# Kernel tuning notes

Measured on AMD Instinct MI355X. Metric: run time of the kernel, lower is better.

The kernel has to match this reference:

```python
import jax, jax.numpy as jnp
import numpy as np


def setup_inputs() -> dict:
    key = jax.random.key(0)
    k1, k2 = jax.random.split(key)
    B, C, H, W, T = 32, 128, 16, 16, 32
    outputs = jax.random.normal(k1, (B, C, H, W, T), dtype=jnp.float32)
    target = (jax.random.uniform(k2, (B, C, H, W, T)) < 0.2).astype(jnp.float32)
    return {"outputs": outputs, "target": target, "n_steps": T, "tau_s": 4}


def _psp(target, tau_s):
    """Leaky integrator over the last (time) axis: syn_t = syn_{t-1}*(1-1/tau) + x_t; out_t = syn_t/tau."""
    tau = jnp.asarray(tau_s, target.dtype)
    decay = 1.0 - 1.0 / tau
    x = jnp.moveaxis(target, -1, 0)  # [T, B, C, H, W]

    def step(syn, x_t):
        syn = syn * decay + x_t
        return syn, syn / tau

    _, syns = jax.lax.scan(step, jnp.zeros(target.shape[:-1], target.dtype), x)
    return jnp.moveaxis(syns, 0, -1)  # [B, C, H, W, T]


def reference(outputs, target, n_steps, tau_s):
    # spike_kernel: delta = outputs - psp(target); loss = 0.5 * sum(delta^2)
    target_psp = _psp(target, tau_s)
    delta = outputs - target_psp
    return 0.5 * jnp.sum(delta * delta)
```

## Files before the change

### kernel.cpp

```cpp
#include <hip/hip_runtime.h>


#define NBLOCKS 2048
#define NTHREADS 256

__global__ __launch_bounds__(NTHREADS) void spike_loss_main(
    const float* __restrict__ outputs,
    const float* __restrict__ target,
    const int* __restrict__ tau_p,
    float* __restrict__ partials,
    int total4)
{
    const float tau = (float)tau_p[0];
    const float d  = 1.0f - 1.0f / tau;
    const float inv_tau = 1.0f / tau;
    const float d2 = d * d;
    const float d3 = d2 * d;
    const float d4 = d2 * d2;
    const float d8 = d4 * d4;
    const float d16 = d8 * d8;

    const int lane = threadIdx.x & 63;
    const int j = lane & 7;

    const float4* __restrict__ t4 = (const float4*)target;
    const float4* __restrict__ o4 = (const float4*)outputs;

    float acc = 0.0f;
    const int stride = gridDim.x * blockDim.x;
    for (int g = blockIdx.x * blockDim.x + threadIdx.x; g < total4; g += stride) {
        float4 x = t4[g];

        float s0 = x.x;
        float s1 = s0 * d + x.y;
        float s2 = s1 * d + x.z;
        float s3 = s2 * d + x.w;

        float S = s3;
        float u;
        u = __shfl_up(S, 1, 8); S += (j >= 1) ? d4  * u : 0.0f;
        u = __shfl_up(S, 2, 8); S += (j >= 2) ? d8  * u : 0.0f;
        u = __shfl_up(S, 4, 8); S += (j >= 4) ? d16 * u : 0.0f;

        float cp = __shfl_up(S, 1, 8);
        cp = (j >= 1) ? cp : 0.0f;
        s0 += cp * d;
        s1 += cp * d2;
        s2 += cp * d3;
        s3 += cp * d4;

        float4 o = o4[g];
        float e0 = o.x - s0 * inv_tau;
        float e1 = o.y - s1 * inv_tau;
        float e2 = o.z - s2 * inv_tau;
        float e3 = o.w - s3 * inv_tau;
        acc += e0 * e0 + e1 * e1 + e2 * e2 + e3 * e3;
    }

    #pragma unroll
    for (int o = 32; o > 0; o >>= 1) acc += __shfl_down(acc, o, 64);

    __shared__ float wsum[NTHREADS / 64];
    if (lane == 0) wsum[threadIdx.x >> 6] = acc;
    __syncthreads();
    if (threadIdx.x == 0) {
        float s = 0.0f;
        #pragma unroll
        for (int w = 0; w < NTHREADS / 64; ++w) s += wsum[w];
        partials[blockIdx.x] = s;
    }
}

__global__ __launch_bounds__(NTHREADS) void spike_loss_final(
    const float* __restrict__ partials, float* __restrict__ out, int n)
{
    float acc = 0.0f;
    for (int i = threadIdx.x; i < n; i += NTHREADS) acc += partials[i];
    #pragma unroll
    for (int o = 32; o > 0; o >>= 1) acc += __shfl_down(acc, o, 64);

    __shared__ float wsum[NTHREADS / 64];
    const int lane = threadIdx.x & 63;
    if (lane == 0) wsum[threadIdx.x >> 6] = acc;
    __syncthreads();
    if (threadIdx.x == 0) {
        float s = 0.0f;
        #pragma unroll
        for (int w = 0; w < NTHREADS / 64; ++w) s += wsum[w];
        out[0] = 0.5f * s;
    }
}

extern "C" void kernel_launch(void* const* d_in, const int* in_sizes, int n_in,
                              void* d_out, int out_size, void* d_ws, size_t ws_size,
                              hipStream_t stream) {
    const float* outputs = (const float*)d_in[0];
    const float* target  = (const float*)d_in[1];
    const int*   tau_p   = (const int*)d_in[3];

    float* partials = (float*)d_ws;
    const int total4 = in_sizes[0] / 4;

    spike_loss_main<<<NBLOCKS, NTHREADS, 0, stream>>>(outputs, target, tau_p, partials, total4);
    spike_loss_final<<<1, NTHREADS, 0, stream>>>(partials, (float*)d_out, NBLOCKS);
}
```

Measured before the change: 51.71 us.

## Unroll loads 8-deep and fuse final reduction via atomicAdd

Batches eight float4 loads per tensor ahead of the scan arithmetic, using a scheduling barrier, to raise memory-level parallelism. It replaces the second reduction kernel with a per-block atomicAdd into the output, which is zeroed by a memset, and turns the lane masks into precomputed FMA weights. This saves a kernel launch and keeps more loads in flight, at the cost of higher register use and a result that depends on the order of atomic additions.

```diff
diff --git a/kernel.cpp b/kernel.cpp
--- a/kernel.cpp
+++ b/kernel.cpp
@@ -3,12 +3,13 @@
 
 #define NBLOCKS 2048
 #define NTHREADS 256
+#define U 8
 
-__global__ __launch_bounds__(NTHREADS) void spike_loss_main(
+__global__ __launch_bounds__(NTHREADS) void spike_loss_fused(
     const float* __restrict__ outputs,
     const float* __restrict__ target,
     const int* __restrict__ tau_p,
-    float* __restrict__ partials,
+    float* __restrict__ out,
     int total4)
 {
     const float tau = (float)tau_p[0];
@@ -23,38 +24,79 @@
     const int lane = threadIdx.x & 63;
     const int j = lane & 7;
 
+    const float w1 = (j >= 1) ? d4  : 0.0f;
+    const float w2 = (j >= 2) ? d8  : 0.0f;
+    const float w4 = (j >= 4) ? d16 : 0.0f;
+    const float c1 = (j >= 1) ? d   : 0.0f;
+    const float c2 = (j >= 1) ? d2  : 0.0f;
+    const float c3 = (j >= 1) ? d3  : 0.0f;
+    const float c4 = (j >= 1) ? d4  : 0.0f;
+
     const float4* __restrict__ t4 = (const float4*)target;
     const float4* __restrict__ o4 = (const float4*)outputs;
 
     float acc = 0.0f;
     const int stride = gridDim.x * blockDim.x;
-    for (int g = blockIdx.x * blockDim.x + threadIdx.x; g < total4; g += stride) {
-        float4 x = t4[g];
+    int g = blockIdx.x * blockDim.x + threadIdx.x;
 
+    for (; g + (U - 1) * stride < total4; g += U * stride) {
+        float4 xv[U], ov[U];
+        #pragma unroll
+        for (int u = 0; u < U; ++u) xv[u] = t4[g + u * stride];
+        #pragma unroll
+        for (int u = 0; u < U; ++u) ov[u] = o4[g + u * stride];
+        __builtin_amdgcn_sched_barrier(0);
+
+        #pragma unroll
+        for (int u = 0; u < U; ++u) {
+            float4 x = xv[u], o = ov[u];
+            float s0 = x.x;
+            float s1 = s0 * d + x.y;
+            float s2 = s1 * d + x.z;
+            float s3 = s2 * d + x.w;
+            float S = s3;
+            float u1 = __shfl_up(S, 1, 8); S = fmaf(w1, u1, S);
+            float u2 = __shfl_up(S, 2, 8); S = fmaf(w2, u2, S);
+            float u4 = __shfl_up(S, 4, 8); S = fmaf(w4, u4, S);
+            float cp = __shfl_up(S, 1, 8);
+            s0 = fmaf(cp, c1, s0);
+            s1 = fmaf(cp, c2, s1);
+            s2 = fmaf(cp, c3, s2);
+            s3 = fmaf(cp, c4, s3);
+
+            float e0 = fmaf(-inv_tau, s0, o.x);
+            float e1 = fmaf(-inv_tau, s1, o.y);
+            float e2 = fmaf(-inv_tau, s2, o.z);
+            float e3 = fmaf(-inv_tau, s3, o.w);
+            acc = fmaf(e0, e0, acc);
+            acc = fmaf(e1, e1, acc);
+            acc = fmaf(e2, e2, acc);
+            acc = fmaf(e3, e3, acc);
+        }
+    }
+    for (; g < total4; g += stride) {
+        float4 x = t4[g], o = o4[g];
         float s0 = x.x;
         float s1 = s0 * d + x.y;
         float s2 = s1 * d + x.z;
         float s3 = s2 * d + x.w;
-
         float S = s3;
-        float u;
-        u = __shfl_up(S, 1, 8); S += (j >= 1) ? d4  * u : 0.0f;
-        u = __shfl_up(S, 2, 8); S += (j >= 2) ? d8  * u : 0.0f;
-        u = __shfl_up(S, 4, 8); S += (j >= 4) ? d16 * u : 0.0f;
-
+        float u1 = __shfl_up(S, 1, 8); S = fmaf(w1, u1, S);
+        float u2 = __shfl_up(S, 2, 8); S = fmaf(w2, u2, S);
+        float u4 = __shfl_up(S, 4, 8); S = fmaf(w4, u4, S);
         float cp = __shfl_up(S, 1, 8);
-        cp = (j >= 1) ? cp : 0.0f;
-        s0 += cp * d;
-        s1 += cp * d2;
-        s2 += cp * d3;
-        s3 += cp * d4;
-
-        float4 o = o4[g];
-        float e0 = o.x - s0 * inv_tau;
-        float e1 = o.y - s1 * inv_tau;
-        float e2 = o.z - s2 * inv_tau;
-        float e3 = o.w - s3 * inv_tau;
-        acc += e0 * e0 + e1 * e1 + e2 * e2 + e3 * e3;
+        s0 = fmaf(cp, c1, s0);
+        s1 = fmaf(cp, c2, s1);
+        s2 = fmaf(cp, c3, s2);
+        s3 = fmaf(cp, c4, s3);
+        float e0 = fmaf(-inv_tau, s0, o.x);
+        float e1 = fmaf(-inv_tau, s1, o.y);
+        float e2 = fmaf(-inv_tau, s2, o.z);
+        float e3 = fmaf(-inv_tau, s3, o.w);
+        acc = fmaf(e0, e0, acc);
+        acc = fmaf(e1, e1, acc);
+        acc = fmaf(e2, e2, acc);
+        acc = fmaf(e3, e3, acc);
     }
 
     #pragma unroll
@@ -67,27 +109,7 @@
         float s = 0.0f;
         #pragma unroll
         for (int w = 0; w < NTHREADS / 64; ++w) s += wsum[w];
-        partials[blockIdx.x] = s;
-    }
-}
-
-__global__ __launch_bounds__(NTHREADS) void spike_loss_final(
-    const float* __restrict__ partials, float* __restrict__ out, int n)
-{
-    float acc = 0.0f;
-    for (int i = threadIdx.x; i < n; i += NTHREADS) acc += partials[i];
-    #pragma unroll
-    for (int o = 32; o > 0; o >>= 1) acc += __shfl_down(acc, o, 64);
-
-    __shared__ float wsum[NTHREADS / 64];
-    const int lane = threadIdx.x & 63;
-    if (lane == 0) wsum[threadIdx.x >> 6] = acc;
-    __syncthreads();
-    if (threadIdx.x == 0) {
-        float s = 0.0f;
-        #pragma unroll
-        for (int w = 0; w < NTHREADS / 64; ++w) s += wsum[w];
-        out[0] = 0.5f * s;
+        atomicAdd(out, 0.5f * s);
     }
 }
 
@@ -98,9 +120,9 @@
     const float* target  = (const float*)d_in[1];
     const int*   tau_p   = (const int*)d_in[3];
 
-    float* partials = (float*)d_ws;
     const int total4 = in_sizes[0] / 4;
 
-    spike_loss_main<<<NBLOCKS, NTHREADS, 0, stream>>>(outputs, target, tau_p, partials, total4);
-    spike_loss_final<<<1, NTHREADS, 0, stream>>>(partials, (float*)d_out, NBLOCKS);
+    hipMemsetAsync(d_out, 0, sizeof(float), stream);
+    spike_loss_fused<<<NBLOCKS, NTHREADS, 0, stream>>>(
+        outputs, target, tau_p, (float*)d_out, total4);
 }
```

Result: slower. 57.22 us (+10.7%).
